# Performance work log

Measured on AMD Instinct MI355X. Metric: run time of the kernel, lower is better.

## Reference

```python
import jax, jax.numpy as jnp
import numpy as np

N_NODES = 200_000
N_UND = 3_200_000        # undirected masked edges
E = 2 * N_UND            # directed edges


def _seg_mean(m, dst, n_nodes):
    # DGL fn.mean: mean over incoming edge messages; zero-in-degree nodes get 0.
    s = jax.ops.segment_sum(m, dst, num_segments=n_nodes)
    deg = jax.ops.segment_sum(jnp.ones((m.shape[0], 1), m.dtype), dst, num_segments=n_nodes)
    return s / jnp.maximum(deg, 1.0)


def setup_inputs() -> dict:
    key = jax.random.key(0)
    ks = jax.random.split(key, 18)
    w = lambda k, s: jax.random.normal(k, s, dtype=jnp.float32) * 0.1
    return {
        'node_feat': jax.random.normal(ks[0], (N_NODES, 7), dtype=jnp.float32),
        'edge_feat': jax.random.normal(ks[1], (E, 4), dtype=jnp.float32),
        'edge_mask': jax.random.normal(ks[2], (N_UND, 1), dtype=jnp.float32),
        'src': jax.random.randint(ks[3], (E,), 0, N_NODES),
        'dst': jax.random.randint(ks[4], (E,), 0, N_NODES),
        'W1a': w(ks[5], (11, 32)), 'b1a': jnp.zeros((32,), jnp.float32),
        'W1b': w(ks[6], (32, 32)), 'b1b': jnp.zeros((32,), jnp.float32),
        'W2a': w(ks[7], (32, 32)), 'b2a': jnp.zeros((32,), jnp.float32),
        'W2b': w(ks[8], (32, 32)), 'b2b': jnp.zeros((32,), jnp.float32),
        'Wm1': w(ks[9], (32, 16)), 'bm1': jnp.zeros((16,), jnp.float32),
        'Wm2': w(ks[10], (16, 2)), 'bm2': jnp.zeros((2,), jnp.float32),
    }


def reference(node_feat, edge_feat, edge_mask, src, dst,
              W1a, b1a, W1b, b1b, W2a, b2a, W2b, b2b, Wm1, bm1, Wm2, bm2):
    n_nodes = node_feat.shape[0]
    relu = jax.nn.relu
    # interleave mask to both edge directions: [m0, m0, m1, m1, ...]
    m_full = jax.nn.sigmoid(jnp.repeat(edge_mask, 2, axis=0))  # [E, 1]
    # layer 1: masked cat(edge_h, src_h) -> mean over dst -> MLP
    msg1 = m_full * jnp.concatenate([edge_feat, node_feat[src]], axis=1)  # [E, 11]
    h = _seg_mean(msg1, dst, n_nodes)                                      # [N, 11]
    h = relu(relu(h @ W1a + b1a) @ W1b + b1b)                              # [N, 32]
    # layer 2: masked src_h -> mean over dst -> MLP
    msg2 = m_full * h[src]                                                 # [E, 32]
    h = _seg_mean(msg2, dst, n_nodes)                                      # [N, 32]
    h = relu(relu(h @ W2a + b2a) @ W2b + b2b)                              # [N, 32]
    # global max pool + readout MLP + softmax (batch_size=1 path)
    g = jnp.max(h, axis=0)                                                 # [32]
    logits = relu(g @ Wm1 + bm1) @ Wm2 + bm2                               # [2]
    return jax.nn.softmax(logits)[None, :]                                 # [1, 2]
```

## Files before the change

### kernel.cpp

```cpp
#include <hip/hip_runtime.h>
#include <hip/hip_fp16.h>
#include <math.h>

#define SCHUNK 1024
#define PMAX   80

__device__ __forceinline__ float sigmoidf_(float x) {
    return 1.0f / (1.0f + __expf(-x));
}

union I2H { int i; __half2 h; };
__device__ __forceinline__ int pack_h2(float a, float b) {
    I2H u; u.h = __floats2half2_rn(a, b); return u.i;
}
__device__ __forceinline__ float2 unpack_h2(int w) {
    I2H u; u.i = w; return __half22float2(u.h);
}

typedef int v4i_nt __attribute__((ext_vector_type(4)));
typedef float v4f_nt __attribute__((ext_vector_type(4)));
__device__ __forceinline__ int4 ldnt16(const int4* p) {
    v4i_nt v = __builtin_nontemporal_load((const v4i_nt*)p);
    return make_int4(v[0], v[1], v[2], v[3]);
}
__device__ __forceinline__ float4 ldnt16f(const float* p) {
    v4f_nt v = __builtin_nontemporal_load((const v4f_nt*)p);
    return make_float4(v[0], v[1], v[2], v[3]);
}

__global__ void hist_rank(const int* __restrict__ dst, int* __restrict__ deg,
                          int* __restrict__ rank, int E) {
    int e = blockIdx.x * blockDim.x + threadIdx.x;
    if (e < E) rank[e] = atomicAdd(&deg[dst[e]], 1);
}

__global__ void scan_part(const int* __restrict__ deg, int* __restrict__ bsum, int N) {
    __shared__ int tot[256];
    int t = threadIdx.x;
    int base = blockIdx.x * SCHUNK + t * 4;
    int s = 0;
    if (base + 3 < N) {
        int4 v = *(const int4*)(deg + base);
        s = v.x + v.y + v.z + v.w;
    } else {
#pragma unroll
        for (int j = 0; j < 4; ++j) if (base + j < N) s += deg[base + j];
    }
    tot[t] = s;
    __syncthreads();
    for (int o = 128; o >= 1; o >>= 1) {
        if (t < o) tot[t] += tot[t + o];
        __syncthreads();
    }
    if (t == 0) bsum[blockIdx.x] = tot[0];
}

__global__ void scan_mid(int* __restrict__ bsum, int* __restrict__ off, int B, int N) {
    __shared__ int tmp[256];
    int t = threadIdx.x;
    int chunk = (B + 255) / 256;
    int lo = t * chunk, hi = min(lo + chunk, B);
    int s = 0;
    for (int i = lo; i < hi; ++i) s += bsum[i];
    tmp[t] = s;
    __syncthreads();
    for (int o = 1; o < 256; o <<= 1) {
        int v = (t >= o) ? tmp[t - o] : 0;
        __syncthreads();
        tmp[t] += v;
        __syncthreads();
    }
    int run = (t == 0) ? 0 : tmp[t - 1];
    for (int i = lo; i < hi; ++i) { int d = bsum[i]; bsum[i] = run; run += d; }
    if (t == 255) off[N] = tmp[255];
}

__global__ void scan_fin(const int* __restrict__ deg, const int* __restrict__ bsum,
                         int* __restrict__ off, int N) {
    __shared__ int tots[256];
    int t = threadIdx.x;
    int base = blockIdx.x * SCHUNK + t * 4;
    int v0 = 0, v1 = 0, v2 = 0, v3 = 0;
    if (base + 3 < N) {
        int4 v = *(const int4*)(deg + base);
        v0 = v.x; v1 = v.y; v2 = v.z; v3 = v.w;
    } else {
        if (base + 0 < N) v0 = deg[base + 0];
        if (base + 1 < N) v1 = deg[base + 1];
        if (base + 2 < N) v2 = deg[base + 2];
        if (base + 3 < N) v3 = deg[base + 3];
    }
    tots[t] = v0 + v1 + v2 + v3;
    __syncthreads();
    for (int o = 1; o < 256; o <<= 1) {
        int v = (t >= o) ? tots[t - o] : 0;
        __syncthreads();
        tots[t] += v;
        __syncthreads();
    }
    int run = bsum[blockIdx.x] + ((t == 0) ? 0 : tots[t - 1]);
    if (base + 0 < N) off[base + 0] = run; run += v0;
    if (base + 1 < N) off[base + 1] = run; run += v1;
    if (base + 2 < N) off[base + 2] = run; run += v2;
    if (base + 3 < N) off[base + 3] = run;
}

__global__ void pack_nodes(const float* __restrict__ nf, int4* __restrict__ nf16, int N) {
    int n = blockIdx.x * blockDim.x + threadIdx.x;
    if (n >= N) return;
    const float* p = nf + (size_t)n * 7;
    int4 w;
    w.x = pack_h2(p[0], p[1]);
    w.y = pack_h2(p[2], p[3]);
    w.z = pack_h2(p[4], p[5]);
    w.w = pack_h2(p[6], 0.0f);
    nf16[n] = w;
}

__global__ void hist_fill_p(const int* __restrict__ dst, const int* __restrict__ src,
                            const float* __restrict__ edge_mask,
                            const float* __restrict__ edge_feat,
                            const float* __restrict__ node_feat,
                            int* __restrict__ deg, int4* __restrict__ recP,
                            int4* __restrict__ nf16, int E, int N) {
    int t = blockIdx.x * blockDim.x + threadIdx.x;
    if (t < N) {
        const float* p = node_feat + (size_t)t * 7;
        int4 w;
        w.x = pack_h2(p[0], p[1]);
        w.y = pack_h2(p[2], p[3]);
        w.z = pack_h2(p[4], p[5]);
        w.w = pack_h2(p[6], 0.0f);
        nf16[t] = w;
    }
    int e0 = blockIdx.x * (blockDim.x << 2) + threadIdx.x;
    int e1 = e0 + blockDim.x;
    int e2 = e1 + blockDim.x;
    int e3 = e2 + blockDim.x;
    bool v0 = e0 < E, v1 = e1 < E, v2 = e2 < E, v3 = e3 < E;

    int d0 = 0, d1 = 0, d2 = 0, d3 = 0;
    int s0 = 0, s1 = 0, s2 = 0, s3 = 0;
    float k0 = 0, k1 = 0, k2 = 0, k3 = 0;
    float4 f0 = {}, f1 = {}, f2 = {}, f3 = {};
    if (v0) { d0 = dst[e0]; s0 = src[e0]; k0 = edge_mask[e0 >> 1]; f0 = ldnt16f(edge_feat + (size_t)e0 * 4); }
    if (v1) { d1 = dst[e1]; s1 = src[e1]; k1 = edge_mask[e1 >> 1]; f1 = ldnt16f(edge_feat + (size_t)e1 * 4); }
    if (v2) { d2 = dst[e2]; s2 = src[e2]; k2 = edge_mask[e2 >> 1]; f2 = ldnt16f(edge_feat + (size_t)e2 * 4); }
    if (v3) { d3 = dst[e3]; s3 = src[e3]; k3 = edge_mask[e3 >> 1]; f3 = ldnt16f(edge_feat + (size_t)e3 * 4); }

    float m0 = sigmoidf_(k0), m1 = sigmoidf_(k1), m2 = sigmoidf_(k2), m3 = sigmoidf_(k3);
    int4 w0, w1, w2, w3;
    w0.x = s0; w0.y = pack_h2(m0 * f0.x, m0 * f0.y); w0.z = pack_h2(m0 * f0.z, m0 * f0.w); w0.w = __float_as_int(m0);
    w1.x = s1; w1.y = pack_h2(m1 * f1.x, m1 * f1.y); w1.z = pack_h2(m1 * f1.z, m1 * f1.w); w1.w = __float_as_int(m1);
    w2.x = s2; w2.y = pack_h2(m2 * f2.x, m2 * f2.y); w2.z = pack_h2(m2 * f2.z, m2 * f2.w); w2.w = __float_as_int(m2);
    w3.x = s3; w3.y = pack_h2(m3 * f3.x, m3 * f3.y); w3.z = pack_h2(m3 * f3.z, m3 * f3.w); w3.w = __float_as_int(m3);

    int r0 = 0, r1 = 0, r2 = 0, r3 = 0;
    if (v0) r0 = atomicAdd(&deg[d0], 1);
    if (v1) r1 = atomicAdd(&deg[d1], 1);
    if (v2) r2 = atomicAdd(&deg[d2], 1);
    if (v3) r3 = atomicAdd(&deg[d3], 1);

    if (v0 && r0 < PMAX) recP[(size_t)d0 * PMAX + r0] = w0;
    if (v1 && r1 < PMAX) recP[(size_t)d1 * PMAX + r1] = w1;
    if (v2 && r2 < PMAX) recP[(size_t)d2 * PMAX + r2] = w2;
    if (v3 && r3 < PMAX) recP[(size_t)d3 * PMAX + r3] = w3;
}

__global__ void agg1_p(const int4* __restrict__ recP, const int* __restrict__ degv,
                       const int4* __restrict__ nf16,
                       const float* __restrict__ W1a, const float* __restrict__ b1a,
                       const float* __restrict__ W1b, const float* __restrict__ b1b,
                       __half* __restrict__ h1h, int N) {
    __shared__ float sW1a[11 * 32], sb1a[32], sW1b[32 * 32], sb1b[32];
    for (int i = threadIdx.x; i < 11 * 32; i += blockDim.x) sW1a[i] = W1a[i];
    for (int i = threadIdx.x; i < 32 * 32; i += blockDim.x) sW1b[i] = W1b[i];
    if (threadIdx.x < 32) { sb1a[threadIdx.x] = b1a[threadIdx.x]; sb1b[threadIdx.x] = b1b[threadIdx.x]; }
    __syncthreads();
    int n = blockIdx.x * (blockDim.x >> 2) + (threadIdx.x >> 2);
    int sub = threadIdx.x & 3;
    int deg = 0;
    size_t start = 0;
    if (n < N) { deg = degv[n]; start = (size_t)n * PMAX; }
    int dd = min(deg, PMAX);
    float x[11];
#pragma unroll
    for (int j = 0; j < 11; ++j) x[j] = 0.0f;
    int i = sub;
    for (; i + 4 < dd; i += 8) {
        int4 r0 = ldnt16(recP + start + i);
        int4 r1 = ldnt16(recP + start + i + 4);
        int4 nw0 = nf16[r0.x];
        int4 nw1 = nf16[r1.x];
        {
            float m = __int_as_float(r0.w);
            float2 e01 = unpack_h2(r0.y), e23 = unpack_h2(r0.z);
            x[0] += e01.x; x[1] += e01.y; x[2] += e23.x; x[3] += e23.y;
            float2 n01 = unpack_h2(nw0.x), n23 = unpack_h2(nw0.y);
            float2 n45 = unpack_h2(nw0.z), n6 = unpack_h2(nw0.w);
            x[4] += m * n01.x; x[5]  += m * n01.y; x[6] += m * n23.x; x[7] += m * n23.y;
            x[8] += m * n45.x; x[9]  += m * n45.y; x[10] += m * n6.x;
        }
        {
            float m = __int_as_float(r1.w);
            float2 e01 = unpack_h2(r1.y), e23 = unpack_h2(r1.z);
            x[0] += e01.x; x[1] += e01.y; x[2] += e23.x; x[3] += e23.y;
            float2 n01 = unpack_h2(nw1.x), n23 = unpack_h2(nw1.y);
            float2 n45 = unpack_h2(nw1.z), n6 = unpack_h2(nw1.w);
            x[4] += m * n01.x; x[5]  += m * n01.y; x[6] += m * n23.x; x[7] += m * n23.y;
            x[8] += m * n45.x; x[9]  += m * n45.y; x[10] += m * n6.x;
        }
    }
    for (; i < dd; i += 4) {
        int4 r = ldnt16(recP + start + i);
        float m = __int_as_float(r.w);
        float2 e01 = unpack_h2(r.y), e23 = unpack_h2(r.z);
        x[0] += e01.x; x[1] += e01.y; x[2] += e23.x; x[3] += e23.y;
        int4 nw = nf16[r.x];
        float2 n01 = unpack_h2(nw.x), n23 = unpack_h2(nw.y);
        float2 n45 = unpack_h2(nw.z), n6 = unpack_h2(nw.w);
        x[4] += m * n01.x; x[5]  += m * n01.y; x[6] += m * n23.x; x[7] += m * n23.y;
        x[8] += m * n45.x; x[9]  += m * n45.y; x[10] += m * n6.x;
    }
#pragma unroll
    for (int j = 0; j < 11; ++j) {
        x[j] += __shfl_xor(x[j], 1);
        x[j] += __shfl_xor(x[j], 2);
    }
    if (n >= N) return;
    float inv = 1.0f / fmaxf((float)deg, 1.0f);
#pragma unroll
    for (int j = 0; j < 11; ++j) x[j] *= inv;
    float hdn[32];
#pragma unroll
    for (int k = 0; k < 32; ++k) {
        float acc = sb1a[k];
#pragma unroll
        for (int j = 0; j < 11; ++j) acc += x[j] * sW1a[j * 32 + k];
        hdn[k] = fmaxf(acc, 0.0f);
    }
    float o[32];
#pragma unroll
    for (int k2 = 0; k2 < 32; ++k2) {
        float acc = sb1b[k2];
#pragma unroll
        for (int k = 0; k < 32; ++k) acc += hdn[k] * sW1b[k * 32 + k2];
        o[k2] = fmaxf(acc, 0.0f);
    }
    int4 w;
    w.x = pack_h2(o[8 * sub + 0], o[8 * sub + 1]);
    w.y = pack_h2(o[8 * sub + 2], o[8 * sub + 3]);
    w.z = pack_h2(o[8 * sub + 4], o[8 * sub + 5]);
    w.w = pack_h2(o[8 * sub + 6], o[8 * sub + 7]);
    ((int4*)(h1h + (size_t)n * 32))[sub] = w;
}

__global__ void agg2_p(const int4* __restrict__ recP, const int* __restrict__ degv,
                       const __half* __restrict__ h1h,
                       const float* __restrict__ W2a, const float* __restrict__ b2a,
                       const float* __restrict__ W2b, const float* __restrict__ b2b,
                       float* __restrict__ gmax, int N) {
    __shared__ float sW2a[32 * 32], sb2a[32], sW2b[32 * 32], sb2b[32];
    __shared__ int smax[32];
    for (int i = threadIdx.x; i < 32 * 32; i += blockDim.x) { sW2a[i] = W2a[i]; sW2b[i] = W2b[i]; }
    if (threadIdx.x < 32) {
        sb2a[threadIdx.x] = b2a[threadIdx.x];
        sb2b[threadIdx.x] = b2b[threadIdx.x];
        smax[threadIdx.x] = 0;
    }
    __syncthreads();
    int n = blockIdx.x * (blockDim.x >> 2) + (threadIdx.x >> 2);
    int sub = threadIdx.x & 3;
    bool valid = (n < N);
    int deg = 0;
    size_t start = 0;
    if (valid) { deg = degv[n]; start = (size_t)n * PMAX; }
    int dd = min(deg, PMAX);
    float x[32];
#pragma unroll
    for (int j = 0; j < 32; ++j) x[j] = 0.0f;
    int i = sub;
    for (; i + 4 < dd; i += 8) {
        int4 r0 = ldnt16(recP + start + i);
        int4 r1 = ldnt16(recP + start + i + 4);
        const int4* hp0 = (const int4*)(h1h + (size_t)r0.x * 32);
        const int4* hp1 = (const int4*)(h1h + (size_t)r1.x * 32);
        int4 g00 = hp0[0], g01 = hp0[1], g02 = hp0[2], g03 = hp0[3];
        int4 g10 = hp1[0], g11 = hp1[1], g12 = hp1[2], g13 = hp1[3];
        {
            float m = __int_as_float(r0.w);
            float2 a, b, c, d;
            a = unpack_h2(g00.x); b = unpack_h2(g00.y); c = unpack_h2(g00.z); d = unpack_h2(g00.w);
            x[0] += m * a.x; x[1] += m * a.y; x[2] += m * b.x; x[3] += m * b.y;
            x[4] += m * c.x; x[5] += m * c.y; x[6] += m * d.x; x[7] += m * d.y;
            a = unpack_h2(g01.x); b = unpack_h2(g01.y); c = unpack_h2(g01.z); d = unpack_h2(g01.w);
            x[8] += m * a.x; x[9] += m * a.y; x[10] += m * b.x; x[11] += m * b.y;
            x[12] += m * c.x; x[13] += m * c.y; x[14] += m * d.x; x[15] += m * d.y;
            a = unpack_h2(g02.x); b = unpack_h2(g02.y); c = unpack_h2(g02.z); d = unpack_h2(g02.w);
            x[16] += m * a.x; x[17] += m * a.y; x[18] += m * b.x; x[19] += m * b.y;
            x[20] += m * c.x; x[21] += m * c.y; x[22] += m * d.x; x[23] += m * d.y;
            a = unpack_h2(g03.x); b = unpack_h2(g03.y); c = unpack_h2(g03.z); d = unpack_h2(g03.w);
            x[24] += m * a.x; x[25] += m * a.y; x[26] += m * b.x; x[27] += m * b.y;
            x[28] += m * c.x; x[29] += m * c.y; x[30] += m * d.x; x[31] += m * d.y;
        }
        {
            float m = __int_as_float(r1.w);
            float2 a, b, c, d;
            a = unpack_h2(g10.x); b = unpack_h2(g10.y); c = unpack_h2(g10.z); d = unpack_h2(g10.w);
            x[0] += m * a.x; x[1] += m * a.y; x[2] += m * b.x; x[3] += m * b.y;
            x[4] += m * c.x; x[5] += m * c.y; x[6] += m * d.x; x[7] += m * d.y;
            a = unpack_h2(g11.x); b = unpack_h2(g11.y); c = unpack_h2(g11.z); d = unpack_h2(g11.w);
            x[8] += m * a.x; x[9] += m * a.y; x[10] += m * b.x; x[11] += m * b.y;
            x[12] += m * c.x; x[13] += m * c.y; x[14] += m * d.x; x[15] += m * d.y;
            a = unpack_h2(g12.x); b = unpack_h2(g12.y); c = unpack_h2(g12.z); d = unpack_h2(g12.w);
            x[16] += m * a.x; x[17] += m * a.y; x[18] += m * b.x; x[19] += m * b.y;
            x[20] += m * c.x; x[21] += m * c.y; x[22] += m * d.x; x[23] += m * d.y;
            a = unpack_h2(g13.x); b = unpack_h2(g13.y); c = unpack_h2(g13.z); d = unpack_h2(g13.w);
            x[24] += m * a.x; x[25] += m * a.y; x[26] += m * b.x; x[27] += m * b.y;
            x[28] += m * c.x; x[29] += m * c.y; x[30] += m * d.x; x[31] += m * d.y;
        }
    }
    for (; i < dd; i += 4) {
        int4 r = ldnt16(recP + start + i);
        float m = __int_as_float(r.w);
        const int4* hp = (const int4*)(h1h + (size_t)r.x * 32);
#pragma unroll
        for (int q = 0; q < 4; ++q) {
            int4 v = hp[q];
            float2 a = unpack_h2(v.x), b = unpack_h2(v.y);
            float2 c = unpack_h2(v.z), d = unpack_h2(v.w);
            x[8 * q + 0] += m * a.x; x[8 * q + 1] += m * a.y;
            x[8 * q + 2] += m * b.x; x[8 * q + 3] += m * b.y;
            x[8 * q + 4] += m * c.x; x[8 * q + 5] += m * c.y;
            x[8 * q + 6] += m * d.x; x[8 * q + 7] += m * d.y;
        }
    }
#pragma unroll
    for (int j = 0; j < 32; ++j) {
        x[j] += __shfl_xor(x[j], 1);
        x[j] += __shfl_xor(x[j], 2);
    }
    float inv = 1.0f / fmaxf((float)deg, 1.0f);
#pragma unroll
    for (int j = 0; j < 32; ++j) x[j] *= inv;
    float hdn[32];
#pragma unroll
    for (int k = 0; k < 32; ++k) {
        float acc = sb2a[k];
#pragma unroll
        for (int j = 0; j < 32; ++j) acc += x[j] * sW2a[j * 32 + k];
        hdn[k] = fmaxf(acc, 0.0f);
    }
    int lane = threadIdx.x & 63;
#pragma unroll
    for (int k2 = 0; k2 < 32; ++k2) {
        float acc = sb2b[k2];
#pragma unroll
        for (int k = 0; k < 32; ++k) acc += hdn[k] * sW2b[k * 32 + k2];
        float v = valid ? fmaxf(acc, 0.0f) : 0.0f;
#pragma unroll
        for (int o = 32; o >= 1; o >>= 1)
            v = fmaxf(v, __shfl_xor(v, o));
        if (lane == 0) atomicMax(&smax[k2], __float_as_int(v));
    }
    __syncthreads();
    if (threadIdx.x < 32) atomicMax((int*)&gmax[threadIdx.x], smax[threadIdx.x]);
}

__global__ void fill_rec16(const int* __restrict__ dst, const int* __restrict__ rank,
                           const int* __restrict__ off,
                           const float* __restrict__ edge_mask,
                           const int* __restrict__ src,
                           const float* __restrict__ edge_feat,
                           int4* __restrict__ rec, int E) {
    int e = blockIdx.x * blockDim.x + threadIdx.x;
    if (e >= E) return;
    int p = off[dst[e]] + rank[e];
    float m = sigmoidf_(edge_mask[e >> 1]);
    float4 ef = ldnt16f(edge_feat + (size_t)e * 4);
    int4 w;
    w.x = src[e];
    w.y = pack_h2(m * ef.x, m * ef.y);
    w.z = pack_h2(m * ef.z, m * ef.w);
    w.w = __float_as_int(m);
    rec[p] = w;
}

__global__ void agg1_16(const int4* __restrict__ rec, const int* __restrict__ off,
                        const int4* __restrict__ nf16,
                        const float* __restrict__ W1a, const float* __restrict__ b1a,
                        const float* __restrict__ W1b, const float* __restrict__ b1b,
                        __half* __restrict__ h1h, int N) {
    __shared__ float sW1a[11 * 32], sb1a[32], sW1b[32 * 32], sb1b[32];
    for (int i = threadIdx.x; i < 11 * 32; i += blockDim.x) sW1a[i] = W1a[i];
    for (int i = threadIdx.x; i < 32 * 32; i += blockDim.x) sW1b[i] = W1b[i];
    if (threadIdx.x < 32) { sb1a[threadIdx.x] = b1a[threadIdx.x]; sb1b[threadIdx.x] = b1b[threadIdx.x]; }
    __syncthreads();
    int n = blockIdx.x * (blockDim.x >> 2) + (threadIdx.x >> 2);
    int sub = threadIdx.x & 3;
    int start = 0, deg = 0;
    if (n < N) { start = off[n]; deg = off[n + 1] - start; }
    float x[11];
#pragma unroll
    for (int j = 0; j < 11; ++j) x[j] = 0.0f;
    for (int i = sub; i < deg; i += 4) {
        int4 r = ldnt16(rec + start + i);
        float m = __int_as_float(r.w);
        float2 e01 = unpack_h2(r.y), e23 = unpack_h2(r.z);
        x[0] += e01.x; x[1] += e01.y; x[2] += e23.x; x[3] += e23.y;
        int4 nw = nf16[r.x];
        float2 n01 = unpack_h2(nw.x), n23 = unpack_h2(nw.y);
        float2 n45 = unpack_h2(nw.z), n6 = unpack_h2(nw.w);
        x[4] += m * n01.x; x[5]  += m * n01.y; x[6] += m * n23.x; x[7] += m * n23.y;
        x[8] += m * n45.x; x[9]  += m * n45.y; x[10] += m * n6.x;
    }
#pragma unroll
    for (int j = 0; j < 11; ++j) {
        x[j] += __shfl_xor(x[j], 1);
        x[j] += __shfl_xor(x[j], 2);
    }
    if (n >= N) return;
    float inv = 1.0f / fmaxf((float)deg, 1.0f);
#pragma unroll
    for (int j = 0; j < 11; ++j) x[j] *= inv;
    float hdn[32];
#pragma unroll
    for (int k = 0; k < 32; ++k) {
        float acc = sb1a[k];
#pragma unroll
        for (int j = 0; j < 11; ++j) acc += x[j] * sW1a[j * 32 + k];
        hdn[k] = fmaxf(acc, 0.0f);
    }
    float o[32];
#pragma unroll
    for (int k2 = 0; k2 < 32; ++k2) {
        float acc = sb1b[k2];
#pragma unroll
        for (int k = 0; k < 32; ++k) acc += hdn[k] * sW1b[k * 32 + k2];
        o[k2] = fmaxf(acc, 0.0f);
    }
    int4 w;
    w.x = pack_h2(o[8 * sub + 0], o[8 * sub + 1]);
    w.y = pack_h2(o[8 * sub + 2], o[8 * sub + 3]);
    w.z = pack_h2(o[8 * sub + 4], o[8 * sub + 5]);
    w.w = pack_h2(o[8 * sub + 6], o[8 * sub + 7]);
    ((int4*)(h1h + (size_t)n * 32))[sub] = w;
}

__global__ void agg2_16(const int4* __restrict__ rec, const int* __restrict__ off,
                        const __half* __restrict__ h1h,
                        const float* __restrict__ W2a, const float* __restrict__ b2a,
                        const float* __restrict__ W2b, const float* __restrict__ b2b,
                        float* __restrict__ gmax, int N) {
    __shared__ float sW2a[32 * 32], sb2a[32], sW2b[32 * 32], sb2b[32];
    __shared__ int smax[32];
    for (int i = threadIdx.x; i < 32 * 32; i += blockDim.x) { sW2a[i] = W2a[i]; sW2b[i] = W2b[i]; }
    if (threadIdx.x < 32) {
        sb2a[threadIdx.x] = b2a[threadIdx.x];
        sb2b[threadIdx.x] = b2b[threadIdx.x];
        smax[threadIdx.x] = 0;
    }
    __syncthreads();
    int n = blockIdx.x * (blockDim.x >> 2) + (threadIdx.x >> 2);
    int sub = threadIdx.x & 3;
    bool valid = (n < N);
    int start = 0, deg = 0;
    if (valid) { start = off[n]; deg = off[n + 1] - start; }
    float x[32];
#pragma unroll
    for (int j = 0; j < 32; ++j) x[j] = 0.0f;
    for (int i = sub; i < deg; i += 4) {
        int4 r = ldnt16(rec + start + i);
        float m = __int_as_float(r.w);
        const int4* hp = (const int4*)(h1h + (size_t)r.x * 32);
#pragma unroll
        for (int q = 0; q < 4; ++q) {
            int4 v = hp[q];
            float2 a = unpack_h2(v.x), b = unpack_h2(v.y);
            float2 c = unpack_h2(v.z), d = unpack_h2(v.w);
            x[8 * q + 0] += m * a.x; x[8 * q + 1] += m * a.y;
            x[8 * q + 2] += m * b.x; x[8 * q + 3] += m * b.y;
            x[8 * q + 4] += m * c.x; x[8 * q + 5] += m * c.y;
            x[8 * q + 6] += m * d.x; x[8 * q + 7] += m * d.y;
        }
    }
#pragma unroll
    for (int j = 0; j < 32; ++j) {
        x[j] += __shfl_xor(x[j], 1);
        x[j] += __shfl_xor(x[j], 2);
    }
    float inv = 1.0f / fmaxf((float)deg, 1.0f);
#pragma unroll
    for (int j = 0; j < 32; ++j) x[j] *= inv;
    float hdn[32];
#pragma unroll
    for (int k = 0; k < 32; ++k) {
        float acc = sb2a[k];
#pragma unroll
        for (int j = 0; j < 32; ++j) acc += x[j] * sW2a[j * 32 + k];
        hdn[k] = fmaxf(acc, 0.0f);
    }
    int lane = threadIdx.x & 63;
#pragma unroll
    for (int k2 = 0; k2 < 32; ++k2) {
        float acc = sb2b[k2];
#pragma unroll
        for (int k = 0; k < 32; ++k) acc += hdn[k] * sW2b[k * 32 + k2];
        float v = valid ? fmaxf(acc, 0.0f) : 0.0f;
#pragma unroll
        for (int o = 32; o >= 1; o >>= 1)
            v = fmaxf(v, __shfl_xor(v, o));
        if (lane == 0) atomicMax(&smax[k2], __float_as_int(v));
    }
    __syncthreads();
    if (threadIdx.x < 32) atomicMax((int*)&gmax[threadIdx.x], smax[threadIdx.x]);
}

__global__ void fill_rec(const int* __restrict__ dst, const int* __restrict__ rank,
                         const int* __restrict__ off,
                         const float* __restrict__ edge_mask,
                         const int* __restrict__ src,
                         int2* __restrict__ rec, int E) {
    int e = blockIdx.x * blockDim.x + threadIdx.x;
    if (e >= E) return;
    int p = off[dst[e]] + rank[e];
    float m = sigmoidf_(edge_mask[e >> 1]);
    int mq = (int)(m * 16384.0f + 0.5f);
    mq = min(mq, 16383);
    unsigned packed = ((unsigned)src[e] << 14) | (unsigned)mq;
    rec[p] = make_int2(e, (int)packed);
}

__global__ void agg1_rec(const int2* __restrict__ rec, const int* __restrict__ off,
                         const float* __restrict__ edge_feat,
                         const float* __restrict__ node_feat,
                         const float* __restrict__ W1a, const float* __restrict__ b1a,
                         const float* __restrict__ W1b, const float* __restrict__ b1b,
                         float* __restrict__ h1, int N) {
    __shared__ float sW1a[11 * 32], sb1a[32], sW1b[32 * 32], sb1b[32];
    for (int i = threadIdx.x; i < 11 * 32; i += blockDim.x) sW1a[i] = W1a[i];
    for (int i = threadIdx.x; i < 32 * 32; i += blockDim.x) sW1b[i] = W1b[i];
    if (threadIdx.x < 32) { sb1a[threadIdx.x] = b1a[threadIdx.x]; sb1b[threadIdx.x] = b1b[threadIdx.x]; }
    __syncthreads();
    int n = blockIdx.x * blockDim.x + threadIdx.x;
    if (n >= N) return;
    int start = off[n];
    int deg = off[n + 1] - start;
    float x[11];
#pragma unroll
    for (int j = 0; j < 11; ++j) x[j] = 0.0f;
    for (int i = 0; i < deg; ++i) {
        int2 r = rec[start + i];
        int e = r.x;
        unsigned packed = (unsigned)r.y;
        int s = (int)(packed >> 14);
        float m = (float)(packed & 16383u) * (1.0f / 16384.0f);
        float4 ef = *(const float4*)(edge_feat + (size_t)e * 4);
        x[0] += m * ef.x; x[1] += m * ef.y; x[2] += m * ef.z; x[3] += m * ef.w;
        const float* nf = node_feat + (size_t)s * 7;
#pragma unroll
        for (int j = 0; j < 7; ++j) x[4 + j] += m * nf[j];
    }
    float inv = 1.0f / fmaxf((float)deg, 1.0f);
#pragma unroll
    for (int j = 0; j < 11; ++j) x[j] *= inv;
    float hdn[32];
#pragma unroll
    for (int k = 0; k < 32; ++k) {
        float acc = sb1a[k];
#pragma unroll
        for (int j = 0; j < 11; ++j) acc += x[j] * sW1a[j * 32 + k];
        hdn[k] = fmaxf(acc, 0.0f);
    }
    float o[32];
#pragma unroll
    for (int k2 = 0; k2 < 32; ++k2) {
        float acc = sb1b[k2];
#pragma unroll
        for (int k = 0; k < 32; ++k) acc += hdn[k] * sW1b[k * 32 + k2];
        o[k2] = fmaxf(acc, 0.0f);
    }
    float4* outp = (float4*)(h1 + (size_t)n * 32);
#pragma unroll
    for (int q = 0; q < 8; ++q)
        outp[q] = make_float4(o[4 * q], o[4 * q + 1], o[4 * q + 2], o[4 * q + 3]);
}

__global__ void agg2_rec(const int2* __restrict__ rec, const int* __restrict__ off,
                         const float* __restrict__ h1,
                         const float* __restrict__ W2a, const float* __restrict__ b2a,
                         const float* __restrict__ W2b, const float* __restrict__ b2b,
                         float* __restrict__ gmax, int N) {
    __shared__ float sW2a[32 * 32], sb2a[32], sW2b[32 * 32], sb2b[32];
    __shared__ int smax[32];
    for (int i = threadIdx.x; i < 32 * 32; i += blockDim.x) { sW2a[i] = W2a[i]; sW2b[i] = W2b[i]; }
    if (threadIdx.x < 32) {
        sb2a[threadIdx.x] = b2a[threadIdx.x];
        sb2b[threadIdx.x] = b2b[threadIdx.x];
        smax[threadIdx.x] = 0;
    }
    __syncthreads();
    int n = blockIdx.x * blockDim.x + threadIdx.x;
    bool valid = (n < N);
    int nn = valid ? n : 0;
    int start = valid ? off[nn] : 0;
    int deg = valid ? (off[nn + 1] - start) : 0;
    float x[32];
#pragma unroll
    for (int j = 0; j < 32; ++j) x[j] = 0.0f;
    for (int i = 0; i < deg; ++i) {
        int2 r = rec[start + i];
        unsigned packed = (unsigned)r.y;
        int s = (int)(packed >> 14);
        float m = (float)(packed & 16383u) * (1.0f / 16384.0f);
        const float4* hp = (const float4*)(h1 + (size_t)s * 32);
#pragma unroll
        for (int q = 0; q < 8; ++q) {
            float4 v = hp[q];
            x[4 * q + 0] += m * v.x;
            x[4 * q + 1] += m * v.y;
            x[4 * q + 2] += m * v.z;
            x[4 * q + 3] += m * v.w;
        }
    }
    float inv = 1.0f / fmaxf((float)deg, 1.0f);
#pragma unroll
    for (int j = 0; j < 32; ++j) x[j] *= inv;
    float hdn[32];
#pragma unroll
    for (int k = 0; k < 32; ++k) {
        float acc = sb2a[k];
#pragma unroll
        for (int j = 0; j < 32; ++j) acc += x[j] * sW2a[j * 32 + k];
        hdn[k] = fmaxf(acc, 0.0f);
    }
    int lane = threadIdx.x & 63;
#pragma unroll
    for (int k2 = 0; k2 < 32; ++k2) {
        float acc = sb2b[k2];
#pragma unroll
        for (int k = 0; k < 32; ++k) acc += hdn[k] * sW2b[k * 32 + k2];
        float v = valid ? fmaxf(acc, 0.0f) : 0.0f;
#pragma unroll
        for (int o = 32; o >= 1; o >>= 1)
            v = fmaxf(v, __shfl_xor(v, o));
        if (lane == 0) atomicMax(&smax[k2], __float_as_int(v));
    }
    __syncthreads();
    if (threadIdx.x < 32) atomicMax((int*)&gmax[threadIdx.x], smax[threadIdx.x]);
}

__global__ void readout(const float* __restrict__ gmax,
                        const float* __restrict__ Wm1, const float* __restrict__ bm1,
                        const float* __restrict__ Wm2, const float* __restrict__ bm2,
                        float* __restrict__ out) {
    __shared__ float p[16];
    int t = threadIdx.x;
    if (t < 16) {
        float acc = bm1[t];
        for (int j = 0; j < 32; ++j) acc += gmax[j] * Wm1[j * 16 + t];
        p[t] = fmaxf(acc, 0.0f);
    }
    __syncthreads();
    if (t == 0) {
        float l0 = bm2[0], l1 = bm2[1];
        for (int k = 0; k < 16; ++k) { l0 += p[k] * Wm2[k * 2]; l1 += p[k] * Wm2[k * 2 + 1]; }
        float mx = fmaxf(l0, l1);
        float e0 = __expf(l0 - mx), e1 = __expf(l1 - mx);
        float s = e0 + e1;
        out[0] = e0 / s;
        out[1] = e1 / s;
    }
}

extern "C" void kernel_launch(void* const* d_in, const int* in_sizes, int n_in,
                              void* d_out, int out_size, void* d_ws, size_t ws_size,
                              hipStream_t stream) {
    const float* node_feat = (const float*)d_in[0];
    const float* edge_feat = (const float*)d_in[1];
    const float* edge_mask = (const float*)d_in[2];
    const int*   src       = (const int*)d_in[3];
    const int*   dst       = (const int*)d_in[4];
    const float* W1a = (const float*)d_in[5];
    const float* b1a = (const float*)d_in[6];
    const float* W1b = (const float*)d_in[7];
    const float* b1b = (const float*)d_in[8];
    const float* W2a = (const float*)d_in[9];
    const float* b2a = (const float*)d_in[10];
    const float* W2b = (const float*)d_in[11];
    const float* b2b = (const float*)d_in[12];
    const float* Wm1 = (const float*)d_in[13];
    const float* bm1 = (const float*)d_in[14];
    const float* Wm2 = (const float*)d_in[15];
    const float* bm2 = (const float*)d_in[16];

    const int N = in_sizes[0] / 7;
    const int E = in_sizes[3];
    const int B = (N + SCHUNK - 1) / SCHUNK;

    {
        int*    deg_i = (int*)d_ws;
        float*  gmax  = (float*)(deg_i + N);
        __half* h1h   = (__half*)(gmax + 32);
        int4*   nf16  = (int4*)(h1h + (size_t)N * 32);
        int4*   recP  = nf16 + N;
        const size_t needP = (size_t)(deg_i + N + 32 - (int*)d_ws) * sizeof(int)
                           + (size_t)N * 32 * sizeof(__half)
                           + (size_t)N * sizeof(int4)
                           + (size_t)N * PMAX * sizeof(int4);
        if (ws_size >= needP) {
            hipMemsetAsync(d_ws, 0, (size_t)(N + 32) * sizeof(int), stream);
            int threadsNeeded = max((E + 3) / 4, N);
            const int gridEF = (threadsNeeded + 255) / 256;
            hist_fill_p<<<gridEF, 256, 0, stream>>>(dst, src, edge_mask, edge_feat,
                                                    node_feat, deg_i, recP, nf16, E, N);
            const int nodeBlocks = (N + 63) / 64;
            agg1_p<<<nodeBlocks, 256, 0, stream>>>(recP, deg_i, nf16,
                                                   W1a, b1a, W1b, b1b, h1h, N);
            agg2_p<<<nodeBlocks, 256, 0, stream>>>(recP, deg_i, h1h,
                                                   W2a, b2a, W2b, b2b, gmax, N);
            readout<<<1, 64, 0, stream>>>(gmax, Wm1, bm1, Wm2, bm2, (float*)d_out);
            return;
        }
    }

    int*   deg_i = (int*)d_ws;
    float* gmax  = (float*)(deg_i + N);
    int*   off   = (int*)(gmax + 32);
    int*   bsum  = off + (N + 1);
    int*   slot  = bsum + (B + 1);

    const size_t slot16 = (size_t)E > (size_t)16 * N ? (size_t)E : (size_t)16 * N;
    int*    rank   = slot;
    __half* h1h    = (__half*)slot;
    int4*   rec16  = (int4*)(slot + slot16);
    int4*   nf16   = rec16 + E;
    const size_t need16 = ((size_t)2 * N + 34 + B + slot16 + (size_t)E * 4 + (size_t)N * 4) * sizeof(int);

    const size_t slot8 = (size_t)E > (size_t)32 * N ? (size_t)E : (size_t)32 * N;
    float* h1f  = (float*)slot;
    int2*  rec8 = (int2*)(slot + slot8);

    hipMemsetAsync(d_ws, 0, (size_t)(N + 32) * sizeof(int), stream);

    hist_rank<<<(E + 255) / 256, 256, 0, stream>>>(dst, deg_i, rank, E);
    scan_part<<<B, 256, 0, stream>>>(deg_i, bsum, N);
    scan_mid<<<1, 256, 0, stream>>>(bsum, off, B, N);
    scan_fin<<<B, 256, 0, stream>>>(deg_i, bsum, off, N);

    if (ws_size >= need16) {
        const int nodeBlocks = (N + 63) / 64;
        pack_nodes<<<(N + 255) / 256, 256, 0, stream>>>(node_feat, nf16, N);
        fill_rec16<<<(E + 255) / 256, 256, 0, stream>>>(dst, rank, off, edge_mask, src,
                                                        edge_feat, rec16, E);
        agg1_16<<<nodeBlocks, 256, 0, stream>>>(rec16, off, nf16,
                                                W1a, b1a, W1b, b1b, h1h, N);
        agg2_16<<<nodeBlocks, 256, 0, stream>>>(rec16, off, h1h,
                                                W2a, b2a, W2b, b2b, gmax, N);
    } else {
        fill_rec<<<(E + 255) / 256, 256, 0, stream>>>(dst, rank, off, edge_mask, src, rec8, E);
        agg1_rec<<<(N + 255) / 256, 256, 0, stream>>>(rec8, off, edge_feat, node_feat,
                                                      W1a, b1a, W1b, b1b, h1f, N);
        agg2_rec<<<(N + 255) / 256, 256, 0, stream>>>(rec8, off, h1f,
                                                      W2a, b2a, W2b, b2b, gmax, N);
    }
    readout<<<1, 64, 0, stream>>>(gmax, Wm1, bm1, Wm2, bm2, (float*)d_out);
}
```

Baseline: 801.5 us.

## Privatize degree histogram per XCD to avoid cross-die atomics

Splits the fused histogram-and-fill kernel into three passes. The first counts degrees in per-XCC private counters using workgroup-scope atomics and records each edge's rank. The second computes per-XCC base offsets for each node, and the third scatters the packed edge records into their slots. The aim is to avoid contended device-scope atomics crossing dies, at the cost of extra passes, an extra rank array, and an 8x larger counter array plus memset. Workgroup-scope atomics on a counter shared across CUs within an XCC rely on that XCC's L2 coherence, which is a correctness risk.

```diff
diff --git a/kernel.cpp b/kernel.cpp
--- a/kernel.cpp
+++ b/kernel.cpp
@@ -4,6 +4,7 @@
 
 #define SCHUNK 1024
 #define PMAX   80
+#define NXCD   8
 
 __device__ __forceinline__ float sigmoidf_(float x) {
     return 1.0f / (1.0f + __expf(-x));
@@ -26,6 +27,16 @@
 __device__ __forceinline__ float4 ldnt16f(const float* p) {
     v4f_nt v = __builtin_nontemporal_load((const v4f_nt*)p);
     return make_float4(v[0], v[1], v[2], v[3]);
+}
+
+__device__ __forceinline__ int xcc_id() {
+    unsigned x;
+    asm volatile("s_getreg_b32 %0, hwreg(HW_REG_XCC_ID)" : "=s"(x));
+    return (int)(x & (NXCD - 1));
+}
+
+__device__ __forceinline__ int l2AtomicInc(int* p) {
+    return __hip_atomic_fetch_add(p, 1, __ATOMIC_RELAXED, __HIP_MEMORY_SCOPE_WORKGROUP);
 }
 
 __global__ void hist_rank(const int* __restrict__ dst, int* __restrict__ deg,
@@ -115,6 +126,61 @@
     w.z = pack_h2(p[4], p[5]);
     w.w = pack_h2(p[6], 0.0f);
     nf16[n] = w;
+}
+
+__global__ void hist_x(const int* __restrict__ dst, const float* __restrict__ node_feat,
+                       int* __restrict__ degx, int* __restrict__ rk,
+                       int4* __restrict__ nf16, int E, int N) {
+    int t = blockIdx.x * blockDim.x + threadIdx.x;
+    if (t < N) {
+        const float* p = node_feat + (size_t)t * 7;
+        int4 w;
+        w.x = pack_h2(p[0], p[1]);
+        w.y = pack_h2(p[2], p[3]);
+        w.z = pack_h2(p[4], p[5]);
+        w.w = pack_h2(p[6], 0.0f);
+        nf16[t] = w;
+    }
+    if (t >= E) return;
+    int d = dst[t];
+    int x = xcc_id();
+    int r = l2AtomicInc(&degx[(size_t)x * N + d]);
+    rk[t] = (x << 16) | r;
+}
+
+__global__ void bases_x(int* __restrict__ degx, int* __restrict__ deg, int N) {
+    int n = blockIdx.x * blockDim.x + threadIdx.x;
+    if (n >= N) return;
+    int run = 0;
+#pragma unroll
+    for (int x = 0; x < NXCD; ++x) {
+        int c = degx[(size_t)x * N + n];
+        degx[(size_t)x * N + n] = run;
+        run += c;
+    }
+    deg[n] = run;
+}
+
+__global__ void fill_x(const int* __restrict__ dst, const int* __restrict__ src,
+                       const float* __restrict__ edge_mask,
+                       const float* __restrict__ edge_feat,
+                       const int* __restrict__ degx , const int* __restrict__ rk,
+                       int4* __restrict__ recP, int E, int N) {
+    int e = blockIdx.x * blockDim.x + threadIdx.x;
+    if (e >= E) return;
+    int d = dst[e];
+    int k = rk[e];
+    int x = k >> 16, r = k & 0xffff;
+    int base = degx[(size_t)x * N + d];
+    int slot = base + r;
+    float m = sigmoidf_(edge_mask[e >> 1]);
+    float4 ef = ldnt16f(edge_feat + (size_t)e * 4);
+    int4 w;
+    w.x = src[e];
+    w.y = pack_h2(m * ef.x, m * ef.y);
+    w.z = pack_h2(m * ef.z, m * ef.w);
+    w.w = __float_as_int(m);
+    if (slot < PMAX) recP[(size_t)d * PMAX + slot] = w;
 }
 
 __global__ void hist_fill_p(const int* __restrict__ dst, const int* __restrict__ src,
@@ -138,7 +204,6 @@
     int e2 = e1 + blockDim.x;
     int e3 = e2 + blockDim.x;
     bool v0 = e0 < E, v1 = e1 < E, v2 = e2 < E, v3 = e3 < E;
-
     int d0 = 0, d1 = 0, d2 = 0, d3 = 0;
     int s0 = 0, s1 = 0, s2 = 0, s3 = 0;
     float k0 = 0, k1 = 0, k2 = 0, k3 = 0;
@@ -147,20 +212,17 @@
     if (v1) { d1 = dst[e1]; s1 = src[e1]; k1 = edge_mask[e1 >> 1]; f1 = ldnt16f(edge_feat + (size_t)e1 * 4); }
     if (v2) { d2 = dst[e2]; s2 = src[e2]; k2 = edge_mask[e2 >> 1]; f2 = ldnt16f(edge_feat + (size_t)e2 * 4); }
     if (v3) { d3 = dst[e3]; s3 = src[e3]; k3 = edge_mask[e3 >> 1]; f3 = ldnt16f(edge_feat + (size_t)e3 * 4); }
-
     float m0 = sigmoidf_(k0), m1 = sigmoidf_(k1), m2 = sigmoidf_(k2), m3 = sigmoidf_(k3);
     int4 w0, w1, w2, w3;
     w0.x = s0; w0.y = pack_h2(m0 * f0.x, m0 * f0.y); w0.z = pack_h2(m0 * f0.z, m0 * f0.w); w0.w = __float_as_int(m0);
     w1.x = s1; w1.y = pack_h2(m1 * f1.x, m1 * f1.y); w1.z = pack_h2(m1 * f1.z, m1 * f1.w); w1.w = __float_as_int(m1);
     w2.x = s2; w2.y = pack_h2(m2 * f2.x, m2 * f2.y); w2.z = pack_h2(m2 * f2.z, m2 * f2.w); w2.w = __float_as_int(m2);
     w3.x = s3; w3.y = pack_h2(m3 * f3.x, m3 * f3.y); w3.z = pack_h2(m3 * f3.z, m3 * f3.w); w3.w = __float_as_int(m3);
-
     int r0 = 0, r1 = 0, r2 = 0, r3 = 0;
     if (v0) r0 = atomicAdd(&deg[d0], 1);
     if (v1) r1 = atomicAdd(&deg[d1], 1);
     if (v2) r2 = atomicAdd(&deg[d2], 1);
     if (v3) r3 = atomicAdd(&deg[d3], 1);
-
     if (v0 && r0 < PMAX) recP[(size_t)d0 * PMAX + r0] = w0;
     if (v1 && r1 < PMAX) recP[(size_t)d1 * PMAX + r1] = w1;
     if (v2 && r2 < PMAX) recP[(size_t)d2 * PMAX + r2] = w2;
@@ -699,6 +761,37 @@
     const int B = (N + SCHUNK - 1) / SCHUNK;
 
     {
+        char* base = (char*)d_ws;
+        size_t offb = 0;
+        int*    degx = (int*)(base + offb);   offb += (size_t)NXCD * N * sizeof(int);
+        float*  gmax = (float*)(base + offb); offb += 32 * sizeof(float);
+        int*    degT = (int*)(base + offb);   offb += (size_t)N * sizeof(int);
+        int4*   nf16 = (int4*)(base + offb);  offb += (size_t)N * sizeof(int4);
+        size_t  rkBytes = (size_t)E * sizeof(int);
+        size_t  h1Bytes = (size_t)N * 32 * sizeof(__half);
+        int*    rk   = (int*)(base + offb);
+        __half* h1h  = (__half*)(base + offb);
+        offb += (rkBytes > h1Bytes ? rkBytes : h1Bytes);
+        int4*   recP = (int4*)(base + offb);  offb += (size_t)N * PMAX * sizeof(int4);
+        const size_t needX = offb;
+        if (ws_size >= needX) {
+            hipMemsetAsync(d_ws, 0, (size_t)NXCD * N * sizeof(int) + 32 * sizeof(float), stream);
+            int threads1 = max(E, N);
+            hist_x<<<(threads1 + 255) / 256, 256, 0, stream>>>(dst, node_feat, degx, rk, nf16, E, N);
+            bases_x<<<(N + 255) / 256, 256, 0, stream>>>(degx, degT, N);
+            fill_x<<<(E + 255) / 256, 256, 0, stream>>>(dst, src, edge_mask, edge_feat,
+                                                        degx, rk, recP, E, N);
+            const int nodeBlocks = (N + 63) / 64;
+            agg1_p<<<nodeBlocks, 256, 0, stream>>>(recP, degT, nf16,
+                                                   W1a, b1a, W1b, b1b, h1h, N);
+            agg2_p<<<nodeBlocks, 256, 0, stream>>>(recP, degT, h1h,
+                                                   W2a, b2a, W2b, b2b, gmax, N);
+            readout<<<1, 64, 0, stream>>>(gmax, Wm1, bm1, Wm2, bm2, (float*)d_out);
+            return;
+        }
+    }
+
+    {
         int*    deg_i = (int*)d_ws;
         float*  gmax  = (float*)(deg_i + N);
         __half* h1h   = (__half*)(gmax + 32);
```

Result: slower. 891.3 us (+11.2%).

## Bin edges by destination bucket before scattering into per-node record slots

Applied to the files above, without the earlier changes.

Replaces the single-pass global-atomic histogram and scatter with a two-stage binning scheme. The first kernel counts edges per bucket of 512 destination nodes using shared-memory atomics, reserves one contiguous range per bucket with a single global atomic per bucket per block, and writes packed records (destination low bits folded into the src word) into per-bucket regions. A second kernel, one block per bucket, reads its region sequentially and scatters records into a node-local slice of recP using shared atomics, then writes the degrees. This aims to cut the global atomic traffic and make the scatter writes cache-local, at the cost of an extra write and read pass over a region of roughly edge-array size, a fixed bucket capacity that silently drops overflow records, and a requirement that N fit in 18 bits.

```diff
diff --git a/kernel.cpp b/kernel.cpp
--- a/kernel.cpp
+++ b/kernel.cpp
@@ -4,6 +4,10 @@
 
 #define SCHUNK 1024
 #define PMAX   80
+#define BSHIFT 9
+#define MAXBKT 1024
+#define BINB   1024
+#define EPT    8
 
 __device__ __forceinline__ float sigmoidf_(float x) {
     return 1.0f / (1.0f + __expf(-x));
@@ -115,6 +119,87 @@
     w.z = pack_h2(p[4], p[5]);
     w.w = pack_h2(p[6], 0.0f);
     nf16[n] = w;
+}
+
+__global__ __launch_bounds__(BINB)
+void binA(const int* __restrict__ dst, const int* __restrict__ src,
+          const float* __restrict__ edge_mask, const float* __restrict__ edge_feat,
+          const float* __restrict__ node_feat,
+          int* __restrict__ bktCnt, int4* __restrict__ region, int4* __restrict__ nf16,
+          int E, int N, int nbkt, int bcap) {
+    __shared__ int cnt[MAXBKT];
+    __shared__ int base[MAXBKT];
+    int t = threadIdx.x;
+    int gt = blockIdx.x * BINB + t;
+    if (gt < N) {
+        const float* p = node_feat + (size_t)gt * 7;
+        int4 w;
+        w.x = pack_h2(p[0], p[1]);
+        w.y = pack_h2(p[2], p[3]);
+        w.z = pack_h2(p[4], p[5]);
+        w.w = pack_h2(p[6], 0.0f);
+        nf16[gt] = w;
+    }
+    for (int i = t; i < nbkt; i += BINB) cnt[i] = 0;
+    __syncthreads();
+    int4 rec[EPT];
+    int  bl[EPT];
+    int e0 = blockIdx.x * (BINB * EPT) + t;
+#pragma unroll
+    for (int j = 0; j < EPT; ++j) {
+        int e = e0 + j * BINB;
+        bl[j] = -1;
+        if (e < E) {
+            int d = dst[e];
+            int s = src[e];
+            float m = sigmoidf_(edge_mask[e >> 1]);
+            float4 ef = ldnt16f(edge_feat + (size_t)e * 4);
+            int b = d >> BSHIFT;
+            int dlo = d & ((1 << BSHIFT) - 1);
+            int lr = atomicAdd(&cnt[b], 1);
+            rec[j].x = (dlo << 18) | s;
+            rec[j].y = pack_h2(m * ef.x, m * ef.y);
+            rec[j].z = pack_h2(m * ef.z, m * ef.w);
+            rec[j].w = __float_as_int(m);
+            bl[j] = (b << 16) | lr;
+        }
+    }
+    __syncthreads();
+    for (int i = t; i < nbkt; i += BINB)
+        base[i] = atomicAdd(&bktCnt[i], cnt[i]);
+    __syncthreads();
+#pragma unroll
+    for (int j = 0; j < EPT; ++j) {
+        if (bl[j] >= 0) {
+            int b = bl[j] >> 16, lr = bl[j] & 0xffff;
+            int pos = base[b] + lr;
+            if (pos < bcap) region[(size_t)b * bcap + pos] = rec[j];
+        }
+    }
+}
+
+__global__ __launch_bounds__(1024)
+void fillS(const int4* __restrict__ region, const int* __restrict__ bktCnt,
+           int4* __restrict__ recP, int* __restrict__ deg, int N, int bcap) {
+    __shared__ int cnt[1 << BSHIFT];
+    int b = blockIdx.x;
+    int t = threadIdx.x;
+    if (t < (1 << BSHIFT)) cnt[t] = 0;
+    __syncthreads();
+    int count = min(bktCnt[b], bcap);
+    const int4* reg = region + (size_t)b * bcap;
+    int n0 = b << BSHIFT;
+    for (int i = t; i < count; i += blockDim.x) {
+        int4 w = ldnt16(reg + i);
+        int dlo = ((unsigned)w.x) >> 18;
+        int r = atomicAdd(&cnt[dlo], 1);
+        if (r < PMAX) {
+            w.x &= 0x3FFFF;
+            recP[(size_t)(n0 + dlo) * PMAX + r] = w;
+        }
+    }
+    __syncthreads();
+    if (t < (1 << BSHIFT) && n0 + t < N) deg[n0 + t] = cnt[t];
 }
 
 __global__ void hist_fill_p(const int* __restrict__ dst, const int* __restrict__ src,
@@ -138,7 +223,6 @@
     int e2 = e1 + blockDim.x;
     int e3 = e2 + blockDim.x;
     bool v0 = e0 < E, v1 = e1 < E, v2 = e2 < E, v3 = e3 < E;
-
     int d0 = 0, d1 = 0, d2 = 0, d3 = 0;
     int s0 = 0, s1 = 0, s2 = 0, s3 = 0;
     float k0 = 0, k1 = 0, k2 = 0, k3 = 0;
@@ -147,20 +231,17 @@
     if (v1) { d1 = dst[e1]; s1 = src[e1]; k1 = edge_mask[e1 >> 1]; f1 = ldnt16f(edge_feat + (size_t)e1 * 4); }
     if (v2) { d2 = dst[e2]; s2 = src[e2]; k2 = edge_mask[e2 >> 1]; f2 = ldnt16f(edge_feat + (size_t)e2 * 4); }
     if (v3) { d3 = dst[e3]; s3 = src[e3]; k3 = edge_mask[e3 >> 1]; f3 = ldnt16f(edge_feat + (size_t)e3 * 4); }
-
     float m0 = sigmoidf_(k0), m1 = sigmoidf_(k1), m2 = sigmoidf_(k2), m3 = sigmoidf_(k3);
     int4 w0, w1, w2, w3;
     w0.x = s0; w0.y = pack_h2(m0 * f0.x, m0 * f0.y); w0.z = pack_h2(m0 * f0.z, m0 * f0.w); w0.w = __float_as_int(m0);
     w1.x = s1; w1.y = pack_h2(m1 * f1.x, m1 * f1.y); w1.z = pack_h2(m1 * f1.z, m1 * f1.w); w1.w = __float_as_int(m1);
     w2.x = s2; w2.y = pack_h2(m2 * f2.x, m2 * f2.y); w2.z = pack_h2(m2 * f2.z, m2 * f2.w); w2.w = __float_as_int(m2);
     w3.x = s3; w3.y = pack_h2(m3 * f3.x, m3 * f3.y); w3.z = pack_h2(m3 * f3.z, m3 * f3.w); w3.w = __float_as_int(m3);
-
     int r0 = 0, r1 = 0, r2 = 0, r3 = 0;
     if (v0) r0 = atomicAdd(&deg[d0], 1);
     if (v1) r1 = atomicAdd(&deg[d1], 1);
     if (v2) r2 = atomicAdd(&deg[d2], 1);
     if (v3) r3 = atomicAdd(&deg[d3], 1);
-
     if (v0 && r0 < PMAX) recP[(size_t)d0 * PMAX + r0] = w0;
     if (v1 && r1 < PMAX) recP[(size_t)d1 * PMAX + r1] = w1;
     if (v2 && r2 < PMAX) recP[(size_t)d2 * PMAX + r2] = w2;
@@ -673,6 +754,8 @@
     }
 }
 
+static inline size_t align16(size_t x) { return (x + 15) & ~(size_t)15; }
+
 extern "C" void kernel_launch(void* const* d_in, const int* in_sizes, int n_in,
                               void* d_out, int out_size, void* d_ws, size_t ws_size,
                               hipStream_t stream) {
@@ -697,6 +780,43 @@
     const int N = in_sizes[0] / 7;
     const int E = in_sizes[3];
     const int B = (N + SCHUNK - 1) / SCHUNK;
+
+    {
+        const int nbkt = (N + (1 << BSHIFT) - 1) >> BSHIFT;
+        if (nbkt <= MAXBKT && N <= (1 << 18)) {
+            int avg = (E + nbkt - 1) / nbkt;
+            int bcap = avg + avg / 8 + 256;
+            char* basep = (char*)d_ws;
+            size_t off0 = 0;
+            int*   bktCnt = (int*)(basep + off0);  off0 += (size_t)(nbkt + 32) * sizeof(int);
+            float* gmax   = (float*)(bktCnt + nbkt);
+            off0 = align16(off0);
+            int*   degS   = (int*)(basep + off0);  off0 += (size_t)N * sizeof(int);
+            off0 = align16(off0);
+            int4*  nf16   = (int4*)(basep + off0); off0 += (size_t)N * sizeof(int4);
+            int4*  recP   = (int4*)(basep + off0); off0 += (size_t)N * PMAX * sizeof(int4);
+            int4*  region = (int4*)(basep + off0);
+            __half* h1h   = (__half*)region;
+            size_t regionBytes = (size_t)nbkt * bcap * sizeof(int4);
+            size_t h1Bytes = (size_t)N * 32 * sizeof(__half);
+            off0 += (regionBytes > h1Bytes ? regionBytes : h1Bytes);
+            const size_t needS = off0;
+            if (ws_size >= needS) {
+                hipMemsetAsync(d_ws, 0, (size_t)(nbkt + 32) * sizeof(int), stream);
+                const int binBlocks = (max(E, N) + BINB * EPT - 1) / (BINB * EPT);
+                binA<<<binBlocks, BINB, 0, stream>>>(dst, src, edge_mask, edge_feat, node_feat,
+                                                     bktCnt, region, nf16, E, N, nbkt, bcap);
+                fillS<<<nbkt, 1024, 0, stream>>>(region, bktCnt, recP, degS, N, bcap);
+                const int nodeBlocks = (N + 63) / 64;
+                agg1_p<<<nodeBlocks, 256, 0, stream>>>(recP, degS, nf16,
+                                                       W1a, b1a, W1b, b1b, h1h, N);
+                agg2_p<<<nodeBlocks, 256, 0, stream>>>(recP, degS, h1h,
+                                                       W2a, b2a, W2b, b2b, gmax, N);
+                readout<<<1, 64, 0, stream>>>(gmax, Wm1, bm1, Wm2, bm2, (float*)d_out);
+                return;
+            }
+        }
+    }
 
     {
         int*    deg_i = (int*)d_ws;
```

New measurement: 668.3 us. 16.6% less time.
